# Kernel optimization log

Hardware: AMD Instinct MI355X
Metric: run time of the kernel (lower is better)

The kernel has to match this reference:

```python
import jax, jax.numpy as jnp
import numpy as np

N = 50000      # nodes
E = 600000     # edges
F_IN = 128     # num_node_features
H = 128        # hidden_channels
C = 10         # num_classes
G = 512        # graphs in batch
EPS = 1e-5


def setup_inputs() -> dict:
    key = jax.random.key(0)
    ks = jax.random.split(key, 12)
    x = jax.random.normal(ks[0], (N, F_IN), dtype=jnp.float32)
    edge_index = jax.random.randint(ks[1], (2, E), 0, N, dtype=jnp.int32)
    batch = jnp.sort(jax.random.randint(ks[2], (N,), 0, G, dtype=jnp.int32))
    s_in = 1.0 / np.sqrt(F_IN)
    s_h = 1.0 / np.sqrt(H)
    W1 = jax.random.uniform(ks[3], (H, F_IN), jnp.float32, -s_in, s_in)
    b1 = jax.random.uniform(ks[4], (H,), jnp.float32, -s_in, s_in)
    W2 = jax.random.uniform(ks[5], (H, H), jnp.float32, -s_h, s_h)
    b2 = jax.random.uniform(ks[6], (H,), jnp.float32, -s_h, s_h)
    W3 = jax.random.uniform(ks[7], (H, H), jnp.float32, -s_h, s_h)
    b3 = jax.random.uniform(ks[8], (H,), jnp.float32, -s_h, s_h)
    Wlin = jax.random.uniform(ks[9], (C, H), jnp.float32, -s_h, s_h)
    blin = jax.random.uniform(ks[10], (C,), jnp.float32, -s_h, s_h)
    return {"x": x, "edge_index": edge_index, "batch": batch,
            "W1": W1, "b1": b1, "W2": W2, "b2": b2, "W3": W3, "b3": b3,
            "Wlin": Wlin, "blin": blin}


def _gcn_norm(edge_index, num_nodes):
    # PyG GCNConv default: add self-loops, symmetric D^-1/2 A D^-1/2 norm
    loop = jnp.arange(num_nodes, dtype=edge_index.dtype)
    src = jnp.concatenate([edge_index[0], loop])
    dst = jnp.concatenate([edge_index[1], loop])
    deg = jax.ops.segment_sum(jnp.ones_like(dst, dtype=jnp.float32), dst,
                              num_segments=num_nodes)
    dinv = jnp.where(deg > 0, jax.lax.rsqrt(deg), 0.0)
    norm = dinv[src] * dinv[dst]  # [E+N]
    return src, dst, norm


def _gcn_conv(x, W, b, src, dst, norm, num_nodes):
    h = x @ W.T                                  # [N, H]
    msg = norm[:, None] * h[src]                 # gather: [E+N, H]
    out = jax.ops.segment_sum(msg, dst, num_segments=num_nodes)  # scatter-add
    return out + b


def _batchnorm(x):
    # BatchNorm1d(affine=False), training mode: batch stats, biased variance
    mu = jnp.mean(x, axis=0)
    var = jnp.mean(jnp.square(x - mu), axis=0)
    return (x - mu) * jax.lax.rsqrt(var + EPS)


def reference(x, edge_index, batch, W1, b1, W2, b2, W3, b3, Wlin, blin):
    src, dst, norm = _gcn_norm(edge_index, N)
    h = _gcn_conv(x, W1, b1, src, dst, norm, N)
    h = jax.nn.relu(_batchnorm(h))
    h = _gcn_conv(h, W2, b2, src, dst, norm, N)
    h = jax.nn.relu(_batchnorm(h))
    h = _gcn_conv(h, W3, b3, src, dst, norm, N)
    # global mean pool over graphs
    sums = jax.ops.segment_sum(h, batch, num_segments=G)
    cnts = jax.ops.segment_sum(jnp.ones((N,), jnp.float32), batch, num_segments=G)
    pooled = sums / jnp.maximum(cnts, 1.0)[:, None]   # [G, H]
    return pooled @ Wlin.T + blin                     # [G, C]
```

## Files before the change

### kernel.cpp

```cpp
#include <hip/hip_runtime.h>
#include <hip/hip_bf16.h>

#define NN 50000
#define NE 600000
#define FD 128
#define NG 512
#define NC 10
static constexpr float EPS_BN = 1e-5f;

typedef __bf16 bf16x8 __attribute__((ext_vector_type(8)));
typedef float f32x4 __attribute__((ext_vector_type(4)));

__device__ __forceinline__ unsigned short f2bf(float x) {
  unsigned u = __float_as_uint(x);
  u = (u + 0x7FFFu + ((u >> 16) & 1u)) >> 16;
  return (unsigned short)u;
}
__device__ __forceinline__ float bf2f(unsigned short h) {
  return __uint_as_float(((unsigned)h) << 16);
}

__global__ __launch_bounds__(256) void k_zero(float4* __restrict__ p) {
  int i = blockIdx.x * 256 + threadIdx.x;
  if (i < 13536) p[i] = make_float4(0.f, 0.f, 0.f, 0.f);
}

#define FILL_CHUNKS 293
#define GRID_E8 (8 * FILL_CHUNKS)
#define DRANGE 6250
__global__ __launch_bounds__(256) void k_deg_scatter(const int* __restrict__ dst, float* __restrict__ deg) {
  int b = blockIdx.x, t = threadIdx.x;
  int g = b & 7;
  int chunk = b >> 3;
  int dlo = g * DRANGE, dhi = dlo + DRANGE;
  int e0 = chunk * 2048;
#pragma unroll
  for (int i = 0; i < 8; ++i) {
    int e = e0 + i * 256 + t;
    if (e < NE) {
      int d = dst[e];
      if (d >= dlo && d < dhi) unsafeAtomicAdd(&deg[d], 1.0f);
    }
  }
}

#define NB 196
__global__ __launch_bounds__(256) void k_bsum(const float* __restrict__ deg, int* __restrict__ bsum) {
  __shared__ int s[256];
  int t = threadIdx.x, i = blockIdx.x * 256 + t;
  s[t] = (i < NN) ? (int)deg[i] : 0;
  __syncthreads();
  for (int o = 128; o > 0; o >>= 1) { if (t < o) s[t] += s[t + o]; __syncthreads(); }
  if (t == 0) bsum[blockIdx.x] = s[0];
}

__global__ __launch_bounds__(256) void k_bscan(const int* __restrict__ bsum, int* __restrict__ bbase) {
  __shared__ int s[256];
  int t = threadIdx.x;
  int v = (t < NB) ? bsum[t] : 0;
  s[t] = v; __syncthreads();
  for (int o = 1; o < 256; o <<= 1) {
    int a = (t >= o) ? s[t - o] : 0; __syncthreads();
    s[t] += a; __syncthreads();
  }
  if (t < NB) bbase[t] = s[t] - v;
}

__global__ __launch_bounds__(256) void k_rowoff_cvt(float* __restrict__ deg, const int* __restrict__ bbase,
                                                    int* __restrict__ row_off, int* __restrict__ cursor,
                                                    const float* __restrict__ W1, const float* __restrict__ W2,
                                                    const float* __restrict__ W3, unsigned short* __restrict__ w2,
                                                    const int* __restrict__ batch, int* __restrict__ gstart) {
  int b = blockIdx.x, t = threadIdx.x;
  if (b < NB) {
    __shared__ int s[256];
    int i = b * 256 + t;
    float dv = (i < NN) ? deg[i] : 0.f;
    int c = (int)dv;
    s[t] = c; __syncthreads();
    for (int o = 1; o < 256; o <<= 1) {
      int a = (t >= o) ? s[t - o] : 0; __syncthreads();
      s[t] += a; __syncthreads();
    }
    int excl = s[t] - c + bbase[b];
    if (i <= NN) {
      row_off[i] = excl;
      if (i < NN) {
        cursor[i] = excl;
        deg[i] = rsqrtf(dv + 1.0f);
      }
    }
  } else if (b < NB + 48) {
    int bb = b - NB;
    int m = bb >> 4;
    const float* W = (m == 0) ? W1 : ((m == 1) ? W2 : W3);
    int i = (bb & 15) * 256 + t;
    float4 v = ((const float4*)W)[i];
    ushort4 hv;
    hv.x = f2bf(v.x); hv.y = f2bf(v.y); hv.z = f2bf(v.z); hv.w = f2bf(v.w);
    int e0 = i * 4, row = e0 >> 7, col = e0 & 127;
    int sc_ = ((col & 120) ^ ((row & 7) << 3)) | (col & 7);
    *(ushort4*)(w2 + m * FD * FD + row * FD + sc_) = hv;
  } else {
    int g = (b - NB - 48) * 256 + t;
    if (g > NG) return;
    int lo = 0, hi = NN;
    while (lo < hi) {
      int mid = (lo + hi) >> 1;
      if (batch[mid] < g) lo = mid + 1; else hi = mid;
    }
    gstart[g] = lo;
  }
}

__global__ __launch_bounds__(256) void k_fill(const int* __restrict__ src, const int* __restrict__ dst,
                                              int* __restrict__ cursor, int* __restrict__ csr_src) {
  int b = blockIdx.x, t = threadIdx.x;
  int g = b & 7;
  int chunk = b >> 3;
  int dlo = g * DRANGE, dhi = dlo + DRANGE;
  int e0 = chunk * 2048;
#pragma unroll
  for (int i = 0; i < 8; ++i) {
    int e = e0 + i * 256 + t;
    if (e < NE) {
      int d = dst[e];
      if (d >= dlo && d < dhi) {
        int pos = atomicAdd(&cursor[d], 1);
        csr_src[pos] = src[e];
      }
    }
  }
}

template <int BN, int F32IN>
__global__ __launch_bounds__(256) void k_gemm(const void* __restrict__ in, const float* __restrict__ bn8,
                                              const unsigned short* __restrict__ wsrc,
                                              const float* __restrict__ dinv,
                                              unsigned short* __restrict__ hb) {
  __shared__ unsigned short w_lds[FD * FD];
  __shared__ float s_musc[2 * FD];
  int t = threadIdx.x;
  {
    const uint4* s4 = (const uint4*)wsrc;
    uint4* d4 = (uint4*)w_lds;
#pragma unroll
    for (int c = 0; c < 8; ++c) d4[c * 256 + t] = s4[c * 256 + t];
  }
  if constexpr (BN != 0) {
    if (t < FD) {
      float s = 0.f, q = 0.f;
#pragma unroll
      for (int c = 0; c < 8; ++c) { s += bn8[c * FD + t]; q += bn8[1024 + c * FD + t]; }
      float m = s * (1.0f / NN);
      float v = fmaxf(q * (1.0f / NN) - m * m, 0.f);
      s_musc[t] = m;
      s_musc[FD + t] = rsqrtf(v + EPS_BN);
    }
  }
  __syncthreads();

  int w = t >> 6, l = t & 63;
  int rt = blockIdx.x * 4 + w;
  if (rt >= NN / 16) return;
  int r = l & 15, g = l >> 4;
  int ko = g * 8;
  f32x4 acc[8];
#pragma unroll
  for (int ct = 0; ct < 8; ++ct) acc[ct] = (f32x4){0.f, 0.f, 0.f, 0.f};

#pragma unroll
  for (int kk = 0; kk < FD; kk += 32) {
    float a0[8];
    if constexpr (F32IN != 0) {
      const float* p0 = (const float*)in + (size_t)(rt * 16 + r) * FD + kk + ko;
      float4 x0 = *(const float4*)p0;
      float4 x1 = *(const float4*)(p0 + 4);
      a0[0] = x0.x; a0[1] = x0.y; a0[2] = x0.z; a0[3] = x0.w;
      a0[4] = x1.x; a0[5] = x1.y; a0[6] = x1.z; a0[7] = x1.w;
    } else {
      uint4 pv = *(const uint4*)((const unsigned short*)in + (size_t)(rt * 16 + r) * FD + kk + ko);
      a0[0] = __uint_as_float(pv.x << 16); a0[1] = __uint_as_float(pv.x & 0xffff0000u);
      a0[2] = __uint_as_float(pv.y << 16); a0[3] = __uint_as_float(pv.y & 0xffff0000u);
      a0[4] = __uint_as_float(pv.z << 16); a0[5] = __uint_as_float(pv.z & 0xffff0000u);
      a0[6] = __uint_as_float(pv.w << 16); a0[7] = __uint_as_float(pv.w & 0xffff0000u);
    }
    if constexpr (BN != 0) {
      const float* mp = s_musc + kk + ko;
      float4 m0 = *(const float4*)mp, m1 = *(const float4*)(mp + 4);
      float4 s0 = *(const float4*)(mp + FD), s1 = *(const float4*)(mp + FD + 4);
      float mu[8] = {m0.x, m0.y, m0.z, m0.w, m1.x, m1.y, m1.z, m1.w};
      float sc[8] = {s0.x, s0.y, s0.z, s0.w, s1.x, s1.y, s1.z, s1.w};
#pragma unroll
      for (int i = 0; i < 8; ++i)
        a0[i] = fmaxf((a0[i] - mu[i]) * sc[i], 0.f);
    }
    bf16x8 ah, al;
#pragma unroll
    for (int i = 0; i < 8; ++i) {
      __bf16 h0 = (__bf16)a0[i];
      ah[i] = h0; al[i] = (__bf16)(a0[i] - (float)h0);
    }
#pragma unroll
    for (int ct = 0; ct < 8; ++ct) {
      int row = ct * 16 + r;
      int idx = row * FD + ((kk + ko) ^ ((r & 7) << 3));
      bf16x8 bh = *(const bf16x8*)(w_lds + idx);
      acc[ct] = __builtin_amdgcn_mfma_f32_16x16x32_bf16(ah, bh, acc[ct], 0, 0, 0);
      acc[ct] = __builtin_amdgcn_mfma_f32_16x16x32_bf16(al, bh, acc[ct], 0, 0, 0);
    }
  }
  float dvr[4];
#pragma unroll
  for (int i = 0; i < 4; ++i) dvr[i] = dinv[rt * 16 + g * 4 + i];
#pragma unroll
  for (int ct = 0; ct < 8; ++ct)
#pragma unroll
    for (int i = 0; i < 4; ++i)
      hb[(size_t)(rt * 16 + g * 4 + i) * FD + ct * 16 + r] = f2bf(dvr[i] * acc[ct][i]);
}

template <int STATS>
__global__ __launch_bounds__(256) void k_agg(const unsigned short* __restrict__ hb,
                                             const float* __restrict__ dinv,
                                             const float* __restrict__ bias, const int* __restrict__ row_off,
                                             const int* __restrict__ csr_src, unsigned short* __restrict__ outb,
                                             float* __restrict__ bn8) {
  int t = threadIdx.x;
  int n = blockIdx.x * 16 + (t >> 4);
  int q = t & 15;
  const uint4* hb4 = (const uint4*)hb;
  float4 acc0, acc1;
  {
    uint4 pv = hb4[(size_t)n * 16 + q];
    acc0.x = __uint_as_float(pv.x << 16); acc0.y = __uint_as_float(pv.x & 0xffff0000u);
    acc0.z = __uint_as_float(pv.y << 16); acc0.w = __uint_as_float(pv.y & 0xffff0000u);
    acc1.x = __uint_as_float(pv.z << 16); acc1.y = __uint_as_float(pv.z & 0xffff0000u);
    acc1.z = __uint_as_float(pv.w << 16); acc1.w = __uint_as_float(pv.w & 0xffff0000u);
  }
  int lo = row_off[n], hi = row_off[n + 1];
  for (int j = lo; j < hi; ++j) {
    int s = csr_src[j];
    uint4 pv = hb4[(size_t)s * 16 + q];
    acc0.x += __uint_as_float(pv.x << 16); acc0.y += __uint_as_float(pv.x & 0xffff0000u);
    acc0.z += __uint_as_float(pv.y << 16); acc0.w += __uint_as_float(pv.y & 0xffff0000u);
    acc1.x += __uint_as_float(pv.z << 16); acc1.y += __uint_as_float(pv.z & 0xffff0000u);
    acc1.z += __uint_as_float(pv.w << 16); acc1.w += __uint_as_float(pv.w & 0xffff0000u);
  }
  float dv = dinv[n];
  float4 b0 = ((const float4*)bias)[q * 2];
  float4 b1v = ((const float4*)bias)[q * 2 + 1];
  float4 o0, o1;
  o0.x = fmaf(dv, acc0.x, b0.x); o0.y = fmaf(dv, acc0.y, b0.y);
  o0.z = fmaf(dv, acc0.z, b0.z); o0.w = fmaf(dv, acc0.w, b0.w);
  o1.x = fmaf(dv, acc1.x, b1v.x); o1.y = fmaf(dv, acc1.y, b1v.y);
  o1.z = fmaf(dv, acc1.z, b1v.z); o1.w = fmaf(dv, acc1.w, b1v.w);
  {
    unsigned short o[8];
    o[0] = f2bf(o0.x); o[1] = f2bf(o0.y); o[2] = f2bf(o0.z); o[3] = f2bf(o0.w);
    o[4] = f2bf(o1.x); o[5] = f2bf(o1.y); o[6] = f2bf(o1.z); o[7] = f2bf(o1.w);
    *(uint4*)(outb + (size_t)n * FD + q * 8) = *(uint4*)o;
  }

  if constexpr (STATS != 0) {
    __shared__ float red_s[16][FD + 4], red_q[16][FD + 4];
    int slot = t >> 4, f = q * 8;
    red_s[slot][f + 0] = o0.x; red_s[slot][f + 1] = o0.y;
    red_s[slot][f + 2] = o0.z; red_s[slot][f + 3] = o0.w;
    red_s[slot][f + 4] = o1.x; red_s[slot][f + 5] = o1.y;
    red_s[slot][f + 6] = o1.z; red_s[slot][f + 7] = o1.w;
    red_q[slot][f + 0] = o0.x * o0.x; red_q[slot][f + 1] = o0.y * o0.y;
    red_q[slot][f + 2] = o0.z * o0.z; red_q[slot][f + 3] = o0.w * o0.w;
    red_q[slot][f + 4] = o1.x * o1.x; red_q[slot][f + 5] = o1.y * o1.y;
    red_q[slot][f + 6] = o1.z * o1.z; red_q[slot][f + 7] = o1.w * o1.w;
    __syncthreads();
    if (t < FD) {
      float s = 0.f, qq = 0.f;
#pragma unroll
      for (int m = 0; m < 16; ++m) { s += red_s[m][t]; qq += red_q[m][t]; }
      int c = (blockIdx.x & 7) * FD + t;
      unsafeAtomicAdd(&bn8[c], s);
      unsafeAtomicAdd(&bn8[1024 + c], qq);
    }
  }
}

__global__ __launch_bounds__(512) void k_poolfinal(const unsigned short* __restrict__ hbB,
                                                   const int* __restrict__ gstart,
                                                   const float* __restrict__ Wlin, const float* __restrict__ blin,
                                                   float* __restrict__ out) {
  __shared__ float ps[4][FD];
  __shared__ float pp[FD];
  int g = blockIdx.x, t = threadIdx.x;
  int part = t >> 7, f = t & 127;
  int lo = gstart[g], hi = gstart[g + 1];
  float s = 0.f;
  for (int n = lo + part; n < hi; n += 4) s += bf2f(hbB[(size_t)n * FD + f]);
  ps[part][f] = s;
  __syncthreads();
  if (t < FD) {
    float tot = ps[0][t] + ps[1][t] + ps[2][t] + ps[3][t];
    pp[t] = tot * (1.0f / fmaxf((float)(hi - lo), 1.0f));
  }
  __syncthreads();
  if (t < NC) {
    float a = blin[t];
    for (int k = 0; k < FD; ++k) a = fmaf(pp[k], Wlin[t * FD + k], a);
    out[g * NC + t] = a;
  }
}

extern "C" void kernel_launch(void* const* d_in, const int* in_sizes, int n_in,
                              void* d_out, int out_size, void* d_ws, size_t ws_size,
                              hipStream_t stream) {
  const float* x    = (const float*)d_in[0];
  const int*   ei   = (const int*)d_in[1];
  const int*   batch= (const int*)d_in[2];
  const float* W1   = (const float*)d_in[3];
  const float* b1   = (const float*)d_in[4];
  const float* W2   = (const float*)d_in[5];
  const float* b2   = (const float*)d_in[6];
  const float* W3   = (const float*)d_in[7];
  const float* b3   = (const float*)d_in[8];
  const float* Wlin = (const float*)d_in[9];
  const float* blin = (const float*)d_in[10];
  float* out = (float*)d_out;
  float* ws  = (float*)d_ws;

  const int* srcI = ei;
  const int* dstI = ei + NE;

  float* deg    = ws;
  float* bnA    = ws + 50048;
  float* bnB    = bnA + 2048;
  int*   csr_src= (int*)(bnB + 2048);
  int*   row_off= csr_src + NE;
  int*   cursor = row_off + 50048;
  int*   gstart = cursor + 50048;
  int*   bsum   = gstart + 1024;
  int*   bbase  = bsum + 256;
  unsigned short* w2  = (unsigned short*)(bbase + 256);
  unsigned short* hb  = w2 + 3 * FD * FD;
  unsigned short* hbB = hb + NN * FD;

  dim3 B(256);
  const int gGemm = (NN / 16 + 3) / 4;
  const int gAgg  = NN / 16;

  k_zero<<<53, B, 0, stream>>>((float4*)ws);
  k_deg_scatter<<<GRID_E8, B, 0, stream>>>(dstI, deg);
  k_bsum<<<NB, B, 0, stream>>>(deg, bsum);
  k_bscan<<<1, B, 0, stream>>>(bsum, bbase);
  k_rowoff_cvt<<<NB + 48 + 3, B, 0, stream>>>(deg, bbase, row_off, cursor,
                                              W1, W2, W3, w2, batch, gstart);
  k_fill<<<GRID_E8, B, 0, stream>>>(srcI, dstI, cursor, csr_src);

  k_gemm<0, 1><<<gGemm, B, 0, stream>>>(x, nullptr, w2, deg, hb);
  k_agg<1><<<gAgg, B, 0, stream>>>(hb, deg, b1, row_off, csr_src, hbB, bnA);

  k_gemm<1, 0><<<gGemm, B, 0, stream>>>(hbB, bnA, w2 + FD * FD, deg, hb);
  k_agg<1><<<gAgg, B, 0, stream>>>(hb, deg, b2, row_off, csr_src, hbB, bnB);

  k_gemm<1, 0><<<gGemm, B, 0, stream>>>(hbB, bnB, w2 + 2 * FD * FD, deg, hb);
  k_agg<0><<<gAgg, B, 0, stream>>>(hb, deg, b3, row_off, csr_src, hbB, nullptr);

  k_poolfinal<<<NG, 512, 0, stream>>>(hbB, gstart, Wlin, blin, out);
}
```

Baseline: 238.2 us.

## Remap aggregation blocks to XCD-local node ranges and fold block scan into rowoff

Aggregation blocks are remapped so consecutive block indices cycle across 8 contiguous node ranges, aiming for per-XCD L2 locality on the row_off, output and CSR data. The separate single-block scan kernel is removed; each row-offset block now computes its base by summing preceding block sums with a wavefront reduction. This saves a launch but adds some redundant reads, and the padded grid introduces idle threads.

```diff
diff --git a/kernel.cpp b/kernel.cpp
--- a/kernel.cpp
+++ b/kernel.cpp
@@ -54,19 +54,7 @@
   if (t == 0) bsum[blockIdx.x] = s[0];
 }
 
-__global__ __launch_bounds__(256) void k_bscan(const int* __restrict__ bsum, int* __restrict__ bbase) {
-  __shared__ int s[256];
-  int t = threadIdx.x;
-  int v = (t < NB) ? bsum[t] : 0;
-  s[t] = v; __syncthreads();
-  for (int o = 1; o < 256; o <<= 1) {
-    int a = (t >= o) ? s[t - o] : 0; __syncthreads();
-    s[t] += a; __syncthreads();
-  }
-  if (t < NB) bbase[t] = s[t] - v;
-}
-
-__global__ __launch_bounds__(256) void k_rowoff_cvt(float* __restrict__ deg, const int* __restrict__ bbase,
+__global__ __launch_bounds__(256) void k_rowoff_cvt(float* __restrict__ deg, const int* __restrict__ bsum,
                                                     int* __restrict__ row_off, int* __restrict__ cursor,
                                                     const float* __restrict__ W1, const float* __restrict__ W2,
                                                     const float* __restrict__ W3, unsigned short* __restrict__ w2,
@@ -74,6 +62,14 @@
   int b = blockIdx.x, t = threadIdx.x;
   if (b < NB) {
     __shared__ int s[256];
+    __shared__ int base_s;
+    if (t < 64) {
+      int acc = 0;
+      for (int i = t; i < b; i += 64) acc += bsum[i];
+#pragma unroll
+      for (int o = 32; o > 0; o >>= 1) acc += __shfl_down(acc, o, 64);
+      if (t == 0) base_s = acc;
+    }
     int i = b * 256 + t;
     float dv = (i < NN) ? deg[i] : 0.f;
     int c = (int)dv;
@@ -82,7 +78,7 @@
       int a = (t >= o) ? s[t - o] : 0; __syncthreads();
       s[t] += a; __syncthreads();
     }
-    int excl = s[t] - c + bbase[b];
+    int excl = s[t] - c + base_s;
     if (i <= NN) {
       row_off[i] = excl;
       if (i < NN) {
@@ -220,6 +216,8 @@
       hb[(size_t)(rt * 16 + g * 4 + i) * FD + ct * 16 + r] = f2bf(dvr[i] * acc[ct][i]);
 }
 
+#define AGG_CHUNKS 391
+#define GRID_AGG (8 * AGG_CHUNKS)
 template <int STATS>
 __global__ __launch_bounds__(256) void k_agg(const unsigned short* __restrict__ hb,
                                              const float* __restrict__ dinv,
@@ -227,35 +225,38 @@
                                              const int* __restrict__ csr_src, unsigned short* __restrict__ outb,
                                              float* __restrict__ bn8) {
   int t = threadIdx.x;
-  int n = blockIdx.x * 16 + (t >> 4);
+  int b = blockIdx.x;
+  int local = (b >> 3) * 16 + (t >> 4);
+  bool alive = local < DRANGE;
+  int n = (b & 7) * DRANGE + local;
   int q = t & 15;
   const uint4* hb4 = (const uint4*)hb;
-  float4 acc0, acc1;
-  {
-    uint4 pv = hb4[(size_t)n * 16 + q];
-    acc0.x = __uint_as_float(pv.x << 16); acc0.y = __uint_as_float(pv.x & 0xffff0000u);
-    acc0.z = __uint_as_float(pv.y << 16); acc0.w = __uint_as_float(pv.y & 0xffff0000u);
-    acc1.x = __uint_as_float(pv.z << 16); acc1.y = __uint_as_float(pv.z & 0xffff0000u);
-    acc1.z = __uint_as_float(pv.w << 16); acc1.w = __uint_as_float(pv.w & 0xffff0000u);
-  }
-  int lo = row_off[n], hi = row_off[n + 1];
-  for (int j = lo; j < hi; ++j) {
-    int s = csr_src[j];
-    uint4 pv = hb4[(size_t)s * 16 + q];
-    acc0.x += __uint_as_float(pv.x << 16); acc0.y += __uint_as_float(pv.x & 0xffff0000u);
-    acc0.z += __uint_as_float(pv.y << 16); acc0.w += __uint_as_float(pv.y & 0xffff0000u);
-    acc1.x += __uint_as_float(pv.z << 16); acc1.y += __uint_as_float(pv.z & 0xffff0000u);
-    acc1.z += __uint_as_float(pv.w << 16); acc1.w += __uint_as_float(pv.w & 0xffff0000u);
-  }
-  float dv = dinv[n];
-  float4 b0 = ((const float4*)bias)[q * 2];
-  float4 b1v = ((const float4*)bias)[q * 2 + 1];
-  float4 o0, o1;
-  o0.x = fmaf(dv, acc0.x, b0.x); o0.y = fmaf(dv, acc0.y, b0.y);
-  o0.z = fmaf(dv, acc0.z, b0.z); o0.w = fmaf(dv, acc0.w, b0.w);
-  o1.x = fmaf(dv, acc1.x, b1v.x); o1.y = fmaf(dv, acc1.y, b1v.y);
-  o1.z = fmaf(dv, acc1.z, b1v.z); o1.w = fmaf(dv, acc1.w, b1v.w);
-  {
+  float4 acc0 = make_float4(0.f, 0.f, 0.f, 0.f), acc1 = make_float4(0.f, 0.f, 0.f, 0.f);
+  float4 o0 = acc0, o1 = acc1;
+  if (alive) {
+    {
+      uint4 pv = hb4[(size_t)n * 16 + q];
+      acc0.x = __uint_as_float(pv.x << 16); acc0.y = __uint_as_float(pv.x & 0xffff0000u);
+      acc0.z = __uint_as_float(pv.y << 16); acc0.w = __uint_as_float(pv.y & 0xffff0000u);
+      acc1.x = __uint_as_float(pv.z << 16); acc1.y = __uint_as_float(pv.z & 0xffff0000u);
+      acc1.z = __uint_as_float(pv.w << 16); acc1.w = __uint_as_float(pv.w & 0xffff0000u);
+    }
+    int lo = row_off[n], hi = row_off[n + 1];
+    for (int j = lo; j < hi; ++j) {
+      int s = csr_src[j];
+      uint4 pv = hb4[(size_t)s * 16 + q];
+      acc0.x += __uint_as_float(pv.x << 16); acc0.y += __uint_as_float(pv.x & 0xffff0000u);
+      acc0.z += __uint_as_float(pv.y << 16); acc0.w += __uint_as_float(pv.y & 0xffff0000u);
+      acc1.x += __uint_as_float(pv.z << 16); acc1.y += __uint_as_float(pv.z & 0xffff0000u);
+      acc1.z += __uint_as_float(pv.w << 16); acc1.w += __uint_as_float(pv.w & 0xffff0000u);
+    }
+    float dv = dinv[n];
+    float4 b0 = ((const float4*)bias)[q * 2];
+    float4 b1v = ((const float4*)bias)[q * 2 + 1];
+    o0.x = fmaf(dv, acc0.x, b0.x); o0.y = fmaf(dv, acc0.y, b0.y);
+    o0.z = fmaf(dv, acc0.z, b0.z); o0.w = fmaf(dv, acc0.w, b0.w);
+    o1.x = fmaf(dv, acc1.x, b1v.x); o1.y = fmaf(dv, acc1.y, b1v.y);
+    o1.z = fmaf(dv, acc1.z, b1v.z); o1.w = fmaf(dv, acc1.w, b1v.w);
     unsigned short o[8];
     o[0] = f2bf(o0.x); o[1] = f2bf(o0.y); o[2] = f2bf(o0.z); o[3] = f2bf(o0.w);
     o[4] = f2bf(o1.x); o[5] = f2bf(o1.y); o[6] = f2bf(o1.z); o[7] = f2bf(o1.w);
@@ -338,31 +339,28 @@
   int*   cursor = row_off + 50048;
   int*   gstart = cursor + 50048;
   int*   bsum   = gstart + 1024;
-  int*   bbase  = bsum + 256;
-  unsigned short* w2  = (unsigned short*)(bbase + 256);
+  unsigned short* w2  = (unsigned short*)(bsum + 256);
   unsigned short* hb  = w2 + 3 * FD * FD;
   unsigned short* hbB = hb + NN * FD;
 
   dim3 B(256);
   const int gGemm = (NN / 16 + 3) / 4;
-  const int gAgg  = NN / 16;
 
   k_zero<<<53, B, 0, stream>>>((float4*)ws);
   k_deg_scatter<<<GRID_E8, B, 0, stream>>>(dstI, deg);
   k_bsum<<<NB, B, 0, stream>>>(deg, bsum);
-  k_bscan<<<1, B, 0, stream>>>(bsum, bbase);
-  k_rowoff_cvt<<<NB + 48 + 3, B, 0, stream>>>(deg, bbase, row_off, cursor,
+  k_rowoff_cvt<<<NB + 48 + 3, B, 0, stream>>>(deg, bsum, row_off, cursor,
                                               W1, W2, W3, w2, batch, gstart);
   k_fill<<<GRID_E8, B, 0, stream>>>(srcI, dstI, cursor, csr_src);
 
   k_gemm<0, 1><<<gGemm, B, 0, stream>>>(x, nullptr, w2, deg, hb);
-  k_agg<1><<<gAgg, B, 0, stream>>>(hb, deg, b1, row_off, csr_src, hbB, bnA);
+  k_agg<1><<<GRID_AGG, B, 0, stream>>>(hb, deg, b1, row_off, csr_src, hbB, bnA);
 
   k_gemm<1, 0><<<gGemm, B, 0, stream>>>(hbB, bnA, w2 + FD * FD, deg, hb);
-  k_agg<1><<<gAgg, B, 0, stream>>>(hb, deg, b2, row_off, csr_src, hbB, bnB);
+  k_agg<1><<<GRID_AGG, B, 0, stream>>>(hb, deg, b2, row_off, csr_src, hbB, bnB);
 
   k_gemm<1, 0><<<gGemm, B, 0, stream>>>(hbB, bnB, w2 + 2 * FD * FD, deg, hb);
-  k_agg<0><<<gAgg, B, 0, stream>>>(hb, deg, b3, row_off, csr_src, hbB, nullptr);
+  k_agg<0><<<GRID_AGG, B, 0, stream>>>(hb, deg, b3, row_off, csr_src, hbB, nullptr);
 
   k_poolfinal<<<NG, 512, 0, stream>>>(hbB, gstart, Wlin, blin, out);
 }
```

Result: no change. 233.7 us (-1.9%).
